# Performance work log

Hardware: AMD Instinct MI355X
Metric: run time of the kernel (lower is better)

The kernel has to match this reference:

```python
import jax, jax.numpy as jnp
import numpy as np

B, N, F_IN = 8, 4096, 128
H0, H1, OUT = 64, 32, 32
DENSITY = 0.004  # avg degree ~16


def setup_inputs() -> dict:
    key = jax.random.key(0)
    ks = jax.random.split(key, 8)
    x = jax.random.normal(ks[0], (B, N, F_IN), dtype=jnp.float32)
    # sparse binary adjacency (graph structure), stored dense as the module does
    adj = (jax.random.uniform(ks[1], (B, N, N)) < DENSITY).astype(jnp.float32)
    def w(k, i, o):
        return jax.random.normal(k, (i, o), dtype=jnp.float32) * (1.0 / np.sqrt(i))
    return {
        "x": x, "adj": adj,
        "Ws0": w(ks[2], F_IN, H0), "Wn0": w(ks[3], F_IN, H0), "b0": jnp.zeros((H0,), jnp.float32),
        "Ws1": w(ks[4], H0, H1),   "Wn1": w(ks[5], H0, H1),   "b1": jnp.zeros((H1,), jnp.float32),
        "Ws2": w(ks[6], H1, OUT),  "Wn2": w(ks[7], H1, OUT),  "b2": jnp.zeros((OUT,), jnp.float32),
    }


def _sage_layer(h, adj, deg_inv, Ws, Wn, b):
    # mean over incoming neighbors: row j of adj selects messages into node j
    neigh = jnp.einsum('bij,bjd->bid', adj, h) * deg_inv  # [B,N,d_in]
    return jax.nn.relu(h @ Ws + neigh @ Wn + b)


def reference(x, adj, Ws0, Wn0, b0, Ws1, Wn1, b1, Ws2, Wn2, b2):
    deg = jnp.sum(adj, axis=-1, keepdims=True)  # [B,N,1] in-degree
    deg_inv = 1.0 / jnp.maximum(deg, 1.0)
    h = _sage_layer(x, adj, deg_inv, Ws0, Wn0, b0)
    h = _sage_layer(h, adj, deg_inv, Ws1, Wn1, b1)
    h = _sage_layer(h, adj, deg_inv, Ws2, Wn2, b2)
    # original flattens to [B*N, out_dim] embeddings
    return h.reshape(B * N, -1)
```

## Files before the change

### kernel.cpp

```cpp
#include <hip/hip_runtime.h>
#include <hip/hip_bf16.h>

#define BN      32768
#define NCOL    4096
#define MAX_NBR 64

#define WS_NBR 0
#define WS_DEG (4*1024*1024)
#define WS_H0  (WS_DEG + 131072)
#define WS_H1  (WS_H0 + 8*1024*1024)

typedef unsigned int u32x4 __attribute__((ext_vector_type(4)));

__global__ __launch_bounds__(256) void fused_csr_layer0_kernel(
    const float* __restrict__ adj,
    const float* __restrict__ x,
    const float* __restrict__ Ws, const float* __restrict__ Wn,
    const float* __restrict__ bias,
    unsigned short* __restrict__ nbr,
    int* __restrict__ deg,
    float* __restrict__ h0)
{
    __shared__ int s_cnt[4];
    __shared__ unsigned short s_list[4][MAX_NBR];
    __shared__ float s_self[4][128];
    __shared__ float s_neigh[4][128];

    const int wave = threadIdx.x >> 6, lane = threadIdx.x & 63;
    const int row  = (((blockIdx.x & 7) << 12) | ((blockIdx.x >> 3) << 2)) + wave;
    const int jbase = row & ~(NCOL - 1);

    if (lane == 0) s_cnt[wave] = 0;
    __syncthreads();

    const u32x4* arow = reinterpret_cast<const u32x4*>(adj + (size_t)row * NCOL);
    #pragma unroll
    for (int t = 0; t < 16; ++t) {
        const u32x4 q = __builtin_nontemporal_load(&arow[t * 64 + lane]);
        if (q.x | q.y | q.z | q.w) {
            const int c4 = (t * 64 + lane) * 4;
            if (q.x) { int p = atomicAdd(&s_cnt[wave], 1);
                       if (p < MAX_NBR) s_list[wave][p] = (unsigned short)(c4    ); }
            if (q.y) { int p = atomicAdd(&s_cnt[wave], 1);
                       if (p < MAX_NBR) s_list[wave][p] = (unsigned short)(c4 + 1); }
            if (q.z) { int p = atomicAdd(&s_cnt[wave], 1);
                       if (p < MAX_NBR) s_list[wave][p] = (unsigned short)(c4 + 2); }
            if (q.w) { int p = atomicAdd(&s_cnt[wave], 1);
                       if (p < MAX_NBR) s_list[wave][p] = (unsigned short)(c4 + 3); }
        }
    }
    __syncthreads();

    const int d   = s_cnt[wave];
    const int cnt = d < MAX_NBR ? d : MAX_NBR;
    const float dinv = 1.0f / (float)(d > 1 ? d : 1);

    if (lane < cnt) nbr[(size_t)row * MAX_NBR + lane] = s_list[wave][lane];
    if (lane == 0) deg[row] = d;

    const float2 sf = *(const float2*)(x + (size_t)row * 128 + 2 * lane);
    float n0 = 0.f, n1 = 0.f;
    for (int t = 0; t < cnt; ++t) {
        const int j = jbase + (int)s_list[wave][t];
        const float2 f = *(const float2*)(x + (size_t)j * 128 + 2 * lane);
        n0 += f.x; n1 += f.y;
    }
    s_self[wave][2 * lane]      = sf.x;
    s_self[wave][2 * lane + 1]  = sf.y;
    s_neigh[wave][2 * lane]     = n0 * dinv;
    s_neigh[wave][2 * lane + 1] = n1 * dinv;

    const int o = lane;
    float acc = 0.f;
    #pragma unroll 8
    for (int k = 0; k < 128; ++k) {
        acc = fmaf(s_self[wave][k],  Ws[k * 64 + o], acc);
        acc = fmaf(s_neigh[wave][k], Wn[k * 64 + o], acc);
    }
    h0[(size_t)row * 64 + o] = fmaxf(acc + bias[o], 0.f);
}

template<int D_IN, int D_OUT>
__global__ __launch_bounds__(256) void gather_layer_kernel(
    const float* __restrict__ hin,
    const unsigned short* __restrict__ nbr,
    const int* __restrict__ deg,
    const float* __restrict__ Ws, const float* __restrict__ Wn,
    const float* __restrict__ bias,
    float* __restrict__ hout)
{
    constexpr int SUB = (D_IN >= 64) ? 1 : (64 / D_IN);
    constexpr int KPL = (D_IN + 63) / 64;
    constexpr int NW  = 4 * SUB;
    __shared__ float s_self[D_IN];
    __shared__ float s_part[NW][D_IN];
    __shared__ float s_neigh[D_IN];

    const int tid  = threadIdx.x;
    const int wave = tid >> 6, lane = tid & 63;
    const int sub  = (D_IN < 64) ? (lane / D_IN) : 0;
    const int sl   = (D_IN < 64) ? (lane % D_IN) : lane;
    const int strm = wave * SUB + sub;
    const int row  = ((blockIdx.x & 7) << 12) | (blockIdx.x >> 3);
    const int jbase = row & ~(NCOL - 1);

    const int d   = deg[row];
    const int cnt = d < MAX_NBR ? d : MAX_NBR;
    const float dinv = 1.0f / (float)(d > 1 ? d : 1);

    int mycol = 0;
    if (lane < cnt) mycol = nbr[(size_t)row * MAX_NBR + lane];

    if (wave == 0) {
        if constexpr (KPL == 2) {
            const float2 f = *(const float2*)(hin + (size_t)row * D_IN + 2 * lane);
            s_self[2 * lane] = f.x; s_self[2 * lane + 1] = f.y;
        } else {
            if (lane < D_IN) s_self[lane] = hin[(size_t)row * D_IN + lane];
        }
    }

    float nv[KPL];
    #pragma unroll
    for (int i = 0; i < KPL; ++i) nv[i] = 0.f;
    for (int t = strm; t < cnt; t += NW) {
        const int j = jbase + __shfl(mycol, t, 64);
        if constexpr (KPL == 2) {
            const float2 f = *(const float2*)(hin + (size_t)j * D_IN + 2 * lane);
            nv[0] += f.x; nv[1] += f.y;
        } else {
            nv[0] += hin[(size_t)j * D_IN + sl];
        }
    }
    if constexpr (KPL == 2) {
        s_part[strm][2 * lane]     = nv[0];
        s_part[strm][2 * lane + 1] = nv[1];
    } else {
        s_part[strm][sl] = nv[0];
    }
    __syncthreads();

    if (tid < D_IN) {
        float s = 0.f;
        #pragma unroll
        for (int p = 0; p < NW; ++p) s += s_part[p][tid];
        s_neigh[tid] = s * dinv;
    }
    __syncthreads();

    if (wave == 0) {
        constexpr int SEG  = 64 / D_OUT;
        constexpr int KSEG = D_IN / SEG;
        const int o = lane % D_OUT, seg = lane / D_OUT;
        float acc = 0.f;
        #pragma unroll 8
        for (int kk = 0; kk < KSEG; ++kk) {
            const int k = seg * KSEG + kk;
            acc = fmaf(s_self[k],  Ws[k * D_OUT + o], acc);
            acc = fmaf(s_neigh[k], Wn[k * D_OUT + o], acc);
        }
        if constexpr (SEG == 2) acc += __shfl_xor(acc, 32, 64);
        if (seg == 0)
            hout[(size_t)row * D_OUT + o] = fmaxf(acc + bias[o], 0.f);
    }
}

extern "C" void kernel_launch(void* const* d_in, const int* in_sizes, int n_in,
                              void* d_out, int out_size, void* d_ws, size_t ws_size,
                              hipStream_t stream) {
    const float* x   = (const float*)d_in[0];
    const float* adj = (const float*)d_in[1];
    const float* Ws0 = (const float*)d_in[2]; const float* Wn0 = (const float*)d_in[3];
    const float* b0  = (const float*)d_in[4];
    const float* Ws1 = (const float*)d_in[5]; const float* Wn1 = (const float*)d_in[6];
    const float* b1  = (const float*)d_in[7];
    const float* Ws2 = (const float*)d_in[8]; const float* Wn2 = (const float*)d_in[9];
    const float* b2  = (const float*)d_in[10];

    char* ws = (char*)d_ws;
    unsigned short* nbr = (unsigned short*)(ws + WS_NBR);
    int*   deg = (int*)(ws + WS_DEG);
    float* h0  = (float*)(ws + WS_H0);
    float* h1  = (float*)(ws + WS_H1);

    fused_csr_layer0_kernel<<<BN / 4, 256, 0, stream>>>(
        adj, x, Ws0, Wn0, b0, nbr, deg, h0);
    gather_layer_kernel<64, 32><<<BN, 256, 0, stream>>>(
        h0, nbr, deg, Ws1, Wn1, b1, h1);
    gather_layer_kernel<32, 32><<<BN, 256, 0, stream>>>(
        h1, nbr, deg, Ws2, Wn2, b2, (float*)d_out);
}
```

Before: 836.4 us.

## Process one adjacency row per block in layer-0 CSR build and gather

Layer 0 now assigns one row per 256-thread block instead of one row per wave. The four waves split the 16KB adjacency scan with all loads issued up front, split the neighbor gather, and reduce partial sums through shared memory. This is meant to raise memory-level parallelism on the dominant dense-adjacency read. In exchange it adds block-wide barriers and shared-atomic contention, and only one wave performs the final 128x64 matvec.

```diff
diff --git a/kernel.cpp b/kernel.cpp
--- a/kernel.cpp
+++ b/kernel.cpp
@@ -21,63 +21,77 @@
     int* __restrict__ deg,
     float* __restrict__ h0)
 {
-    __shared__ int s_cnt[4];
-    __shared__ unsigned short s_list[4][MAX_NBR];
-    __shared__ float s_self[4][128];
-    __shared__ float s_neigh[4][128];
-
-    const int wave = threadIdx.x >> 6, lane = threadIdx.x & 63;
-    const int row  = (((blockIdx.x & 7) << 12) | ((blockIdx.x >> 3) << 2)) + wave;
+    __shared__ int s_cnt;
+    __shared__ unsigned short s_list[MAX_NBR];
+    __shared__ float s_self[128];
+    __shared__ float s_part[4][128];
+    __shared__ float s_neigh[128];
+
+    const int tid  = threadIdx.x;
+    const int wave = tid >> 6, lane = tid & 63;
+    const int row  = ((blockIdx.x & 7) << 12) | (blockIdx.x >> 3);
     const int jbase = row & ~(NCOL - 1);
 
-    if (lane == 0) s_cnt[wave] = 0;
+    if (tid == 0) s_cnt = 0;
     __syncthreads();
 
     const u32x4* arow = reinterpret_cast<const u32x4*>(adj + (size_t)row * NCOL);
+    u32x4 q[4];
     #pragma unroll
-    for (int t = 0; t < 16; ++t) {
-        const u32x4 q = __builtin_nontemporal_load(&arow[t * 64 + lane]);
-        if (q.x | q.y | q.z | q.w) {
-            const int c4 = (t * 64 + lane) * 4;
-            if (q.x) { int p = atomicAdd(&s_cnt[wave], 1);
-                       if (p < MAX_NBR) s_list[wave][p] = (unsigned short)(c4    ); }
-            if (q.y) { int p = atomicAdd(&s_cnt[wave], 1);
-                       if (p < MAX_NBR) s_list[wave][p] = (unsigned short)(c4 + 1); }
-            if (q.z) { int p = atomicAdd(&s_cnt[wave], 1);
-                       if (p < MAX_NBR) s_list[wave][p] = (unsigned short)(c4 + 2); }
-            if (q.w) { int p = atomicAdd(&s_cnt[wave], 1);
-                       if (p < MAX_NBR) s_list[wave][p] = (unsigned short)(c4 + 3); }
-        }
-    }
-    __syncthreads();
-
-    const int d   = s_cnt[wave];
+    for (int t = 0; t < 4; ++t)
+        q[t] = __builtin_nontemporal_load(&arow[(wave * 4 + t) * 64 + lane]);
+    float2 sf;
+    if (wave == 0) sf = *(const float2*)(x + (size_t)row * 128 + 2 * lane);
+
+    #pragma unroll
+    for (int t = 0; t < 4; ++t) {
+        if (q[t].x | q[t].y | q[t].z | q[t].w) {
+            const int c4 = ((wave * 4 + t) * 64 + lane) * 4;
+            if (q[t].x) { int p = atomicAdd(&s_cnt, 1);
+                          if (p < MAX_NBR) s_list[p] = (unsigned short)(c4    ); }
+            if (q[t].y) { int p = atomicAdd(&s_cnt, 1);
+                          if (p < MAX_NBR) s_list[p] = (unsigned short)(c4 + 1); }
+            if (q[t].z) { int p = atomicAdd(&s_cnt, 1);
+                          if (p < MAX_NBR) s_list[p] = (unsigned short)(c4 + 2); }
+            if (q[t].w) { int p = atomicAdd(&s_cnt, 1);
+                          if (p < MAX_NBR) s_list[p] = (unsigned short)(c4 + 3); }
+        }
+    }
+    if (wave == 0) { s_self[2 * lane] = sf.x; s_self[2 * lane + 1] = sf.y; }
+    __syncthreads();
+
+    const int d   = s_cnt;
     const int cnt = d < MAX_NBR ? d : MAX_NBR;
     const float dinv = 1.0f / (float)(d > 1 ? d : 1);
 
-    if (lane < cnt) nbr[(size_t)row * MAX_NBR + lane] = s_list[wave][lane];
-    if (lane == 0) deg[row] = d;
-
-    const float2 sf = *(const float2*)(x + (size_t)row * 128 + 2 * lane);
+    if (tid < cnt) nbr[(size_t)row * MAX_NBR + tid] = s_list[tid];
+    if (tid == 0) deg[row] = d;
+
     float n0 = 0.f, n1 = 0.f;
-    for (int t = 0; t < cnt; ++t) {
-        const int j = jbase + (int)s_list[wave][t];
+    for (int t = wave; t < cnt; t += 4) {
+        const int j = jbase + (int)s_list[t];
         const float2 f = *(const float2*)(x + (size_t)j * 128 + 2 * lane);
         n0 += f.x; n1 += f.y;
     }
-    s_self[wave][2 * lane]      = sf.x;
-    s_self[wave][2 * lane + 1]  = sf.y;
-    s_neigh[wave][2 * lane]     = n0 * dinv;
-    s_neigh[wave][2 * lane + 1] = n1 * dinv;
-
-    const int o = lane;
-    float acc = 0.f;
-    #pragma unroll 8
-    for (int k = 0; k < 128; ++k) {
-        acc = fmaf(s_self[wave][k],  Ws[k * 64 + o], acc);
-        acc = fmaf(s_neigh[wave][k], Wn[k * 64 + o], acc);
-    }
-    h0[(size_t)row * 64 + o] = fmaxf(acc + bias[o], 0.f);
+    s_part[wave][2 * lane]     = n0;
+    s_part[wave][2 * lane + 1] = n1;
+    __syncthreads();
+
+    if (tid < 128)
+        s_neigh[tid] = (s_part[0][tid] + s_part[1][tid] +
+                        s_part[2][tid] + s_part[3][tid]) * dinv;
+    __syncthreads();
+
+    if (wave == 0) {
+        const int o = lane;
+        float acc = 0.f;
+        #pragma unroll 8
+        for (int k = 0; k < 128; ++k) {
+            acc = fmaf(s_self[k],  Ws[k * 64 + o], acc);
+            acc = fmaf(s_neigh[k], Wn[k * 64 + o], acc);
+        }
+        h0[(size_t)row * 64 + o] = fmaxf(acc + bias[o], 0.f);
+    }
 }
 
 template<int D_IN, int D_OUT>
@@ -183,7 +197,7 @@
     float* h0  = (float*)(ws + WS_H0);
     float* h1  = (float*)(ws + WS_H1);
 
-    fused_csr_layer0_kernel<<<BN / 4, 256, 0, stream>>>(
+    fused_csr_layer0_kernel<<<BN, 256, 0, stream>>>(
         adj, x, Ws0, Wn0, b0, nbr, deg, h0);
     gather_layer_kernel<64, 32><<<BN, 256, 0, stream>>>(
         h0, nbr, deg, Ws1, Wn1, b1, h1);
```

After: 828.5 us. About the same (-0.9%).

## Batch adjacency loads and share weight loads across rows in layer-0 GEMV

Applied to the files above, without the earlier changes.

The adjacency scan in the fused layer-0 kernel now issues eight 16-byte loads per batch before scanning them, drops the nontemporal hint and removes the block barriers around the scan. The aim is to keep more memory requests in flight on the 512 MB dense adjacency stream. The per-row GEMV is split so each wave covers a 32-wide k-slice for all four rows in the block. Each weight load is then reused across four rows, and the partial sums are combined through shared memory. This costs one extra shared buffer, two barriers and more registers per thread, which may lower occupancy.

```diff
diff --git a/kernel.cpp b/kernel.cpp
--- a/kernel.cpp
+++ b/kernel.cpp
@@ -9,8 +9,6 @@
 #define WS_DEG (4*1024*1024)
 #define WS_H0  (WS_DEG + 131072)
 #define WS_H1  (WS_H0 + 8*1024*1024)
-
-typedef unsigned int u32x4 __attribute__((ext_vector_type(4)));
 
 __global__ __launch_bounds__(256) void fused_csr_layer0_kernel(
     const float* __restrict__ adj,
@@ -23,34 +21,39 @@
 {
     __shared__ int s_cnt[4];
     __shared__ unsigned short s_list[4][MAX_NBR];
-    __shared__ float s_self[4][128];
-    __shared__ float s_neigh[4][128];
+    __shared__ alignas(16) float s_self[4][128];
+    __shared__ alignas(16) float s_neigh[4][128];
+    __shared__ float s_gemv[4][4][64];
 
     const int wave = threadIdx.x >> 6, lane = threadIdx.x & 63;
     const int row  = (((blockIdx.x & 7) << 12) | ((blockIdx.x >> 3) << 2)) + wave;
     const int jbase = row & ~(NCOL - 1);
 
     if (lane == 0) s_cnt[wave] = 0;
-    __syncthreads();
-
-    const u32x4* arow = reinterpret_cast<const u32x4*>(adj + (size_t)row * NCOL);
-    #pragma unroll
-    for (int t = 0; t < 16; ++t) {
-        const u32x4 q = __builtin_nontemporal_load(&arow[t * 64 + lane]);
-        if (q.x | q.y | q.z | q.w) {
-            const int c4 = (t * 64 + lane) * 4;
-            if (q.x) { int p = atomicAdd(&s_cnt[wave], 1);
-                       if (p < MAX_NBR) s_list[wave][p] = (unsigned short)(c4    ); }
-            if (q.y) { int p = atomicAdd(&s_cnt[wave], 1);
-                       if (p < MAX_NBR) s_list[wave][p] = (unsigned short)(c4 + 1); }
-            if (q.z) { int p = atomicAdd(&s_cnt[wave], 1);
-                       if (p < MAX_NBR) s_list[wave][p] = (unsigned short)(c4 + 2); }
-            if (q.w) { int p = atomicAdd(&s_cnt[wave], 1);
-                       if (p < MAX_NBR) s_list[wave][p] = (unsigned short)(c4 + 3); }
-        }
-    }
-    __syncthreads();
-
+
+    const uint4* arow = reinterpret_cast<const uint4*>(adj + (size_t)row * NCOL);
+    #pragma unroll
+    for (int g = 0; g < 2; ++g) {
+        uint4 q[8];
+        #pragma unroll
+        for (int t = 0; t < 8; ++t) q[t] = arow[(g * 8 + t) * 64 + lane];
+        #pragma unroll
+        for (int t = 0; t < 8; ++t) {
+            if (q[t].x | q[t].y | q[t].z | q[t].w) {
+                const int c4 = ((g * 8 + t) * 64 + lane) * 4;
+                if (q[t].x) { int p = atomicAdd(&s_cnt[wave], 1);
+                              if (p < MAX_NBR) s_list[wave][p] = (unsigned short)(c4    ); }
+                if (q[t].y) { int p = atomicAdd(&s_cnt[wave], 1);
+                              if (p < MAX_NBR) s_list[wave][p] = (unsigned short)(c4 + 1); }
+                if (q[t].z) { int p = atomicAdd(&s_cnt[wave], 1);
+                              if (p < MAX_NBR) s_list[wave][p] = (unsigned short)(c4 + 2); }
+                if (q[t].w) { int p = atomicAdd(&s_cnt[wave], 1);
+                              if (p < MAX_NBR) s_list[wave][p] = (unsigned short)(c4 + 3); }
+            }
+        }
+    }
+
+    const float2 sf = *(const float2*)(x + (size_t)row * 128 + 2 * lane);
     const int d   = s_cnt[wave];
     const int cnt = d < MAX_NBR ? d : MAX_NBR;
     const float dinv = 1.0f / (float)(d > 1 ? d : 1);
@@ -58,7 +61,6 @@
     if (lane < cnt) nbr[(size_t)row * MAX_NBR + lane] = s_list[wave][lane];
     if (lane == 0) deg[row] = d;
 
-    const float2 sf = *(const float2*)(x + (size_t)row * 128 + 2 * lane);
     float n0 = 0.f, n1 = 0.f;
     for (int t = 0; t < cnt; ++t) {
         const int j = jbase + (int)s_list[wave][t];
@@ -69,15 +71,36 @@
     s_self[wave][2 * lane + 1]  = sf.y;
     s_neigh[wave][2 * lane]     = n0 * dinv;
     s_neigh[wave][2 * lane + 1] = n1 * dinv;
-
-    const int o = lane;
-    float acc = 0.f;
-    #pragma unroll 8
-    for (int k = 0; k < 128; ++k) {
-        acc = fmaf(s_self[wave][k],  Ws[k * 64 + o], acc);
-        acc = fmaf(s_neigh[wave][k], Wn[k * 64 + o], acc);
-    }
-    h0[(size_t)row * 64 + o] = fmaxf(acc + bias[o], 0.f);
+    __syncthreads();
+
+    float acc[4] = { 0.f, 0.f, 0.f, 0.f };
+    const int k0 = wave * 32;
+    #pragma unroll
+    for (int gg = 0; gg < 8; ++gg) {
+        const int k = k0 + gg * 4;
+        float w_s[4], w_n[4];
+        #pragma unroll
+        for (int u = 0; u < 4; ++u) {
+            w_s[u] = Ws[(k + u) * 64 + lane];
+            w_n[u] = Wn[(k + u) * 64 + lane];
+        }
+        #pragma unroll
+        for (int r = 0; r < 4; ++r) {
+            const float4 sv = *(const float4*)&s_self[r][k];
+            const float4 nv = *(const float4*)&s_neigh[r][k];
+            acc[r] = fmaf(sv.x, w_s[0], acc[r]);  acc[r] = fmaf(nv.x, w_n[0], acc[r]);
+            acc[r] = fmaf(sv.y, w_s[1], acc[r]);  acc[r] = fmaf(nv.y, w_n[1], acc[r]);
+            acc[r] = fmaf(sv.z, w_s[2], acc[r]);  acc[r] = fmaf(nv.z, w_n[2], acc[r]);
+            acc[r] = fmaf(sv.w, w_s[3], acc[r]);  acc[r] = fmaf(nv.w, w_n[3], acc[r]);
+        }
+    }
+    #pragma unroll
+    for (int r = 0; r < 4; ++r) s_gemv[wave][r][lane] = acc[r];
+    __syncthreads();
+
+    const float v = s_gemv[0][wave][lane] + s_gemv[1][wave][lane] +
+                    s_gemv[2][wave][lane] + s_gemv[3][wave][lane] + bias[lane];
+    h0[(size_t)row * 64 + lane] = fmaxf(v, 0.f);
 }
 
 template<int D_IN, int D_OUT>
```

New measurement: 810.5 us. 3.1% less time.
